# Kernel tuning notes

Hardware: AMD Instinct MI355X
Metric: run time of the kernel (lower is better)

Reference implementation:

```python
import jax, jax.numpy as jnp
import numpy as np

B, IMG, D, HEADS, L, PC, PF, OUT = 8, 128, 128, 4, 2, 8, 4, 32
HC = IMG // PC; NC = HC * HC          # 16x16 -> 256 coarse tokens
HF = IMG // PF; NF = HF * HF          # 32x32 -> 1024 fine tokens


def _ln(x, g, b):
    m = x.mean(-1, keepdims=True)
    v = x.var(-1, keepdims=True)
    return (x - m) * jax.lax.rsqrt(v + 1e-5) * g + b


def _conv(x, w, b, pad):
    y = jax.lax.conv_general_dilated(x, w, (1, 1), ((pad, pad), (pad, pad)),
                                     dimension_numbers=('NCHW', 'OIHW', 'NCHW'))
    return y + b[None, :, None, None]


def _bilinear_ac(x, oh, ow):  # F.interpolate(mode='bilinear', align_corners=True)
    _, _, H, W = x.shape
    ys = jnp.linspace(0.0, H - 1.0, oh)
    xs = jnp.linspace(0.0, W - 1.0, ow)
    y0 = jnp.floor(ys).astype(jnp.int32); y1 = jnp.minimum(y0 + 1, H - 1); wy = (ys - y0)[:, None]
    x0 = jnp.floor(xs).astype(jnp.int32); x1 = jnp.minimum(x0 + 1, W - 1); wx = (xs - x0)[None, :]
    g = lambda yi, xi: x[:, :, yi][:, :, :, xi]
    return (g(y0, x0) * (1 - wy) * (1 - wx) + g(y0, x1) * (1 - wy) * wx
            + g(y1, x0) * wy * (1 - wx) + g(y1, x1) * wy * wx)


def _patchify(x, p):  # F.unfold with kernel=stride=p, in_chans=1
    b, _, h, w = x.shape
    return x.reshape(b, h // p, p, w // p, p).transpose(0, 1, 3, 2, 4).reshape(b, (h // p) * (w // p), p * p)


def _forward(x, Wpc, bpc, Wpf, bpf, type_embed, ln1_g, ln1_b, Wqkv, Wo, bo,
             ln2_g, ln2_b, W1, b1, W2, b2, dWc, dbc, dWf, dbf, fW1, fb1, fW2, fb2):
    Bx = x.shape[0]
    # ---- multi-scale patch embed ----
    coarse = _patchify(x, PC) @ Wpc + bpc + type_embed[0]   # [B,NC,D]
    fine = _patchify(x, PF) @ Wpf + bpf                     # [B,NF,D]
    # ---- edge map: sobel -> avgpool(4) -> threshold at per-image mean ----
    gray = x.mean(1, keepdims=True)
    kx = jnp.array([[[[-1, 0, 1], [-2, 0, 2], [-1, 0, 1]]]], x.dtype)
    ky = jnp.array([[[[-1, -2, -1], [0, 0, 0], [1, 2, 1]]]], x.dtype)
    sx = _conv(gray, kx, jnp.zeros((1,), x.dtype), 1)
    sy = _conv(gray, ky, jnp.zeros((1,), x.dtype), 1)
    e = jnp.sqrt(sx ** 2 + sy ** 2)
    e = e.reshape(Bx, 1, IMG // 4, 4, IMG // 4, 4).mean((3, 5))  # [B,1,32,32] == fine grid
    mask_flat = (e > e.mean((2, 3), keepdims=True)).reshape(Bx, NF)
    # ---- static-shape analogue of per-sample masked gather + pad_sequence:
    # stable sort puts edge tokens first (original pixel order preserved), pads are zeros
    order = jnp.argsort(jnp.logical_not(mask_flat), axis=1, stable=True)   # [B,NF]
    mask_sorted = jnp.take_along_axis(mask_flat, order, 1)
    fine_sorted = jnp.take_along_axis(fine, order[..., None], 1) * mask_sorted[..., None]
    fine_sorted = fine_sorted + type_embed[1]   # type embed added to pads too (as in torch)
    tokens = jnp.concatenate([coarse, fine_sorted], axis=1)   # [B,N,D]
    N = NC + NF
    hd = D // HEADS
    scale = hd ** -0.5
    # ---- encoder blocks (pre-LN attn + MLP, irregular-token path) ----
    for l in range(L):
        y = _ln(tokens, ln1_g[l], ln1_b[l])
        qkv = (y @ Wqkv[l]).reshape(Bx, N, 3, HEADS, hd).transpose(2, 0, 3, 1, 4)
        q, k, v = qkv[0], qkv[1], qkv[2]
        attn = jax.nn.softmax(jnp.einsum('bhqd,bhkd->bhqk', q, k) * scale, axis=-1)
        o = jnp.einsum('bhqk,bhkd->bhqd', attn, v).transpose(0, 2, 1, 3).reshape(Bx, N, D)
        tokens = tokens + o @ Wo[l] + bo[l]
        y = _ln(tokens, ln2_g[l], ln2_b[l])
        tokens = tokens + jax.nn.gelu(y @ W1[l] + b1[l], approximate=False) @ W2[l] + b2[l]
    # ---- multi-scale decoder ----
    c = (tokens[:, :NC] @ dWc + dbc).reshape(Bx, HC, HC, 1).transpose(0, 3, 1, 2)
    c_up = _bilinear_ac(c, OUT, OUT)
    feats = (tokens[:, NC:] @ dWf + dbf) * mask_sorted[..., None]   # pads stay zero
    inv = jnp.argsort(order, axis=1)                                # scatter back to pixel order
    f_flat = jnp.take_along_axis(feats, inv[..., None], 1)          # [B,NF,1]
    f_map = f_flat.reshape(Bx, HF, HF, 1).transpose(0, 3, 1, 2)
    f_up = _bilinear_ac(f_map, OUT, OUT)
    fused = jnp.concatenate([c_up, f_up], axis=1)
    h = jax.nn.relu(_conv(fused, fW1, fb1, 1))
    return _conv(h, fW2, fb2, 1)   # [B,1,32,32]


def setup_inputs() -> dict:
    key = jax.random.key(0)
    ks = jax.random.split(key, 16)
    n = lambda k, shape: jax.random.normal(k, shape, jnp.float32) * 0.02
    z = lambda *shape: jnp.zeros(shape, jnp.float32)
    return {
        'x': jax.random.normal(ks[0], (B, 1, IMG, IMG), jnp.float32),
        'Wpc': n(ks[1], (PC * PC, D)), 'bpc': z(D),
        'Wpf': n(ks[2], (PF * PF, D)), 'bpf': z(D),
        'type_embed': n(ks[3], (2, D)),
        'ln1_g': jnp.ones((L, D), jnp.float32), 'ln1_b': z(L, D),
        'Wqkv': n(ks[4], (L, D, 3 * D)),
        'Wo': n(ks[5], (L, D, D)), 'bo': z(L, D),
        'ln2_g': jnp.ones((L, D), jnp.float32), 'ln2_b': z(L, D),
        'W1': n(ks[6], (L, D, 2 * D)), 'b1': z(L, 2 * D),
        'W2': n(ks[7], (L, 2 * D, D)), 'b2': z(L, D),
        'dWc': n(ks[8], (D, 1)), 'dbc': z(1),
        'dWf': n(ks[9], (D, 1)), 'dbf': z(1),
        'fW1': n(ks[10], (2, 2, 3, 3)) * 10.0, 'fb1': z(2),
        'fW2': n(ks[11], (1, 2, 3, 3)) * 10.0, 'fb2': z(1),
    }


def reference(x, Wpc, bpc, Wpf, bpf, type_embed, ln1_g, ln1_b, Wqkv, Wo, bo,
              ln2_g, ln2_b, W1, b1, W2, b2, dWc, dbc, dWf, dbf, fW1, fb1, fW2, fb2):
    return _forward(x, Wpc, bpc, Wpf, bpf, type_embed, ln1_g, ln1_b, Wqkv, Wo, bo,
                    ln2_g, ln2_b, W1, b1, W2, b2, dWc, dbc, dWf, dbf, fW1, fb1, fW2, fb2)
```

## Files before the change

### kernel.cpp

```cpp
#include <hip/hip_runtime.h>
#include <math.h>

#define Bx 8
#define IMG 128
#define DD 128
#define HEADS 4
#define LL 2
#define PCc 8
#define PFf 4
#define HCc 16
#define NCc 256
#define HFf 32
#define NFf 1024
#define NTOK 1280
#define HD 32
#define SPLIT 4
#define NQT 20

typedef __attribute__((ext_vector_type(8))) short short8;
typedef __attribute__((ext_vector_type(4))) float f32x4;

__device__ __forceinline__ short f2bf(float f) {
  unsigned u = __builtin_bit_cast(unsigned, f);
  u += 0x7FFF + ((u >> 16) & 1);
  return (short)(u >> 16);
}
__device__ __forceinline__ float bf2f(short s) {
  unsigned u = ((unsigned)(unsigned short)s) << 16;
  return __builtin_bit_cast(float, u);
}

__global__ __launch_bounds__(128) void k_coarse(const float* __restrict__ x,
    const float* __restrict__ Wpc, const float* __restrict__ bpc,
    const float* __restrict__ te, float* __restrict__ tokens) {
  int blk = blockIdx.x;
  int b = blk / NCc, t = blk % NCc;
  int hc = t / HCc, wc = t % HCc;
  int d = threadIdx.x;
  __shared__ float patch[PCc * PCc];
  if (d < PCc * PCc) {
    int pi = d / PCc, pj = d % PCc;
    patch[d] = x[(b * IMG + hc * PCc + pi) * IMG + wc * PCc + pj];
  }
  __syncthreads();
  float acc = bpc[d] + te[d];
  #pragma unroll 8
  for (int i = 0; i < PCc * PCc; ++i) acc += patch[i] * Wpc[i * DD + d];
  tokens[(size_t)(b * NTOK + t) * DD + d] = acc;
}

__global__ __launch_bounds__(256) void k_sobel(const float* __restrict__ x,
    float* __restrict__ e) {
  int blk = blockIdx.x;
  int b = blk >> 6, tile = blk & 63;
  int ty = tile >> 3, tx = tile & 7;
  int t = threadIdx.x;
  int ly = t >> 4, lx = t & 15;
  int py = ty * 16 + ly, px = tx * 16 + lx;
  const float* img = x + (size_t)b * IMG * IMG;
  float v[3][3];
  #pragma unroll
  for (int ky = 0; ky < 3; ++ky)
    #pragma unroll
    for (int kx = 0; kx < 3; ++kx) {
      int yy = py + ky - 1, xx = px + kx - 1;
      v[ky][kx] = (yy >= 0 && yy < IMG && xx >= 0 && xx < IMG)
                      ? img[yy * IMG + xx] : 0.f;
    }
  float gx = -v[0][0] + v[0][2] - 2.f * v[1][0] + 2.f * v[1][2] - v[2][0] + v[2][2];
  float gy = -v[0][0] - 2.f * v[0][1] - v[0][2] + v[2][0] + 2.f * v[2][1] + v[2][2];
  __shared__ float sm[256];
  sm[t] = sqrtf(gx * gx + gy * gy);
  __syncthreads();
  if (t < 16) {
    int cy = t >> 2, cx = t & 3;
    float s = 0.f;
    #pragma unroll
    for (int dy = 0; dy < 4; ++dy)
      #pragma unroll
      for (int dx = 0; dx < 4; ++dx) s += sm[(cy * 4 + dy) * 16 + cx * 4 + dx];
    e[b * NFf + (ty * 4 + cy) * 32 + tx * 4 + cx] = s * (1.f / 16.f);
  }
}

__global__ __launch_bounds__(1024) void k_edge_sort(const float* __restrict__ e,
    int* __restrict__ order, int* __restrict__ inv, float* __restrict__ msort) {
  int b = blockIdx.x;
  int t = threadIdx.x;
  int lane = t & 63, wave = t >> 6;
  float ev = e[b * NFf + t];
  __shared__ float wsum[16];
  __shared__ int wcnt[16];
  float r = ev;
  #pragma unroll
  for (int o = 32; o > 0; o >>= 1) r += __shfl_xor(r, o, 64);
  if (lane == 0) wsum[wave] = r;
  __syncthreads();
  float tot = 0.f;
  #pragma unroll
  for (int i = 0; i < 16; ++i) tot += wsum[i];
  float mean = tot * (1.f / 1024.f);
  int m = (ev > mean) ? 1 : 0;
  unsigned long long bal = __ballot(m);
  if (lane == 0) wcnt[wave] = __popcll(bal);
  __syncthreads();
  int wbase = 0, total = 0;
  #pragma unroll
  for (int i = 0; i < 16; ++i) {
    int c = wcnt[i];
    if (i < wave) wbase += c;
    total += c;
  }
  unsigned long long below = (lane == 63) ? ~0ULL : ((1ULL << (lane + 1)) - 1);
  int incl = __popcll(bal & below);
  int eb = wbase + incl - m;
  int pos = m ? eb : (total + t - eb);
  order[b * NFf + pos] = t;
  inv[b * NFf + t] = pos;
  msort[b * NFf + pos] = (float)m;
}

__global__ __launch_bounds__(128) void k_fine(const float* __restrict__ x,
    const float* __restrict__ Wpf, const float* __restrict__ bpf,
    const float* __restrict__ te, const int* __restrict__ inv,
    const float* __restrict__ msort, float* __restrict__ tokens) {
  int blk = blockIdx.x;
  int b = blk / NFf, t = blk % NFf;
  int hf = t / HFf, wf = t % HFf;
  int d = threadIdx.x;
  __shared__ float patch[PFf * PFf];
  if (d < PFf * PFf) {
    int pi = d / PFf, pj = d % PFf;
    patch[d] = x[(b * IMG + hf * PFf + pi) * IMG + wf * PFf + pj];
  }
  __syncthreads();
  float acc = bpf[d];
  #pragma unroll
  for (int i = 0; i < PFf * PFf; ++i) acc += patch[i] * Wpf[i * DD + d];
  int pos = inv[b * NFf + t];
  float mk = msort[b * NFf + pos];
  tokens[(size_t)(b * NTOK + NCc + pos) * DD + d] = acc * mk + te[DD + d];
}

__global__ __launch_bounds__(256) void k_prep_w(const float* __restrict__ Wqkv,
    const float* __restrict__ Wo, const float* __restrict__ W1,
    const float* __restrict__ W2, short* __restrict__ WtQKV,
    short* __restrict__ WtO, short* __restrict__ Wt1, short* __restrict__ Wt2) {
  int idx = blockIdx.x * 256 + threadIdx.x;
  int l = idx / 131072, r = idx % 131072;
  const float* src; short* dst; int N, off;
  if (r < 49152)      { src = Wqkv + l * 49152; dst = WtQKV + l * 49152; N = 384; off = r; }
  else if (r < 65536) { src = Wo + l * 16384;  dst = WtO + l * 16384;  N = 128; off = r - 49152; }
  else if (r < 98304) { src = W1 + l * 32768;  dst = Wt1 + l * 32768;  N = 256; off = r - 65536; }
  else                { src = W2 + l * 32768;  dst = Wt2 + l * 32768;  N = 128; off = r - 98304; }
  int k = off / N, n = off % N;
  int K = (r >= 98304) ? 256 : 128;
  dst[(size_t)n * K + k] = f2bf(src[off]);
}

__global__ __launch_bounds__(256) void k_ln_bf16(const float* __restrict__ inp,
    const float* __restrict__ g, const float* __restrict__ bb,
    short* __restrict__ outp) {
  int row = blockIdx.x * 4 + (threadIdx.x >> 6);
  int lane = threadIdx.x & 63;
  float2 v = ((const float2*)(inp + (size_t)row * DD))[lane];
  float s = v.x + v.y;
  #pragma unroll
  for (int o = 32; o > 0; o >>= 1) s += __shfl_xor(s, o, 64);
  float mean = s * (1.f / 128.f);
  float cx = v.x - mean, cy = v.y - mean;
  float q = cx * cx + cy * cy;
  #pragma unroll
  for (int o = 32; o > 0; o >>= 1) q += __shfl_xor(q, o, 64);
  float rstd = rsqrtf(q * (1.f / 128.f) + 1e-5f);
  float2 gg = ((const float2*)g)[lane];
  float2 bv = ((const float2*)bb)[lane];
  int p = (int)(unsigned short)f2bf(cx * rstd * gg.x + bv.x)
        | ((int)(unsigned short)f2bf(cy * rstd * gg.y + bv.y) << 16);
  ((int*)(outp + (size_t)row * DD))[lane] = p;
}

__global__ __launch_bounds__(256) void k_gemm_mfma(const short* __restrict__ A,
    const short* __restrict__ Wt, const float* __restrict__ bias,
    float* __restrict__ Cf, short* __restrict__ Cb, int K, int N, int do_gelu) {
  __shared__ short Alds[64 * 128];
  __shared__ short Blds[64 * 128];
  int row0 = blockIdx.x * 64, col0 = blockIdx.y * 64;
  int t = threadIdx.x;
  int lane = t & 63, w = t >> 6;
  int m = lane & 15, quad = lane >> 4;
  int lrow = lane >> 4, jphys = lane & 15;
  f32x4 zero = {0.f, 0.f, 0.f, 0.f};
  f32x4 acc[4] = {zero, zero, zero, zero};

  for (int kb = 0; kb < K; kb += 128) {
    __syncthreads();
    #pragma unroll
    for (int j = 0; j < 4; ++j) {
      int c = j * 4 + w;
      int r = c * 4 + lrow;
      int jlog = jphys ^ (r & 15);
      __builtin_amdgcn_global_load_lds(
          (const unsigned*)&A[(size_t)(row0 + r) * K + kb + jlog * 8],
          (unsigned*)&Alds[c * 512], 16, 0, 0);
      __builtin_amdgcn_global_load_lds(
          (const unsigned*)&Wt[(size_t)(col0 + r) * K + kb + jlog * 8],
          (unsigned*)&Blds[c * 512], 16, 0, 0);
    }
    __syncthreads();
    #pragma unroll
    for (int ks = 0; ks < 4; ++ks) {
      int pc = ((quad + ks * 4) ^ m) * 8;
      short8 af = *(const short8*)&Alds[(w * 16 + m) * 128 + pc];
      #pragma unroll
      for (int nt = 0; nt < 4; ++nt) {
        short8 bf = *(const short8*)&Blds[(nt * 16 + m) * 128 + pc];
        acc[nt] = __builtin_amdgcn_mfma_f32_16x16x32_bf16(af, bf, acc[nt], 0, 0, 0);
      }
    }
  }
  #pragma unroll
  for (int nt = 0; nt < 4; ++nt) {
    int col = col0 + nt * 16 + m;
    float bv = bias ? bias[col] : 0.f;
    #pragma unroll
    for (int r = 0; r < 4; ++r) {
      int row = row0 + w * 16 + quad * 4 + r;
      float v = acc[nt][r] + bv;
      if (do_gelu) v = 0.5f * v * (1.f + erff(v * 0.70710678118654752f));
      if (Cf) Cf[(size_t)row * N + col] += v;
      else    Cb[(size_t)row * N + col] = f2bf(v);
    }
  }
}

__global__ __launch_bounds__(256) void k_gemm_wo(const short* __restrict__ Opart,
    const float* __restrict__ Lpart, const short* __restrict__ Wt,
    const float* __restrict__ bias, float* __restrict__ Cf) {
  __shared__ short Alds[64 * 136];
  __shared__ short Blds[64 * 128];
  int row0 = blockIdx.x * 64, col0 = blockIdx.y * 64;
  int b = row0 / NTOK, qt = (row0 / 64) % NQT;
  int t = threadIdx.x;
  int lane = t & 63, w = t >> 6;
  int m = lane & 15, quad = lane >> 4;
  int lrow = lane >> 4, jphys = lane & 15;
  f32x4 zero = {0.f, 0.f, 0.f, 0.f};
  f32x4 acc[4] = {zero, zero, zero, zero};

  #pragma unroll
  for (int it = 0; it < 4; ++it) {
    int idx = t + it * 256;
    int q = idx >> 4, j = idx & 15;
    int hh = j >> 2, dd = (j & 3) * 8;
    size_t pb = ((size_t)(b * HEADS + hh) * NQT + qt) * SPLIT;
    float L = Lpart[(pb + 0) * 64 + q] + Lpart[(pb + 1) * 64 + q]
            + Lpart[(pb + 2) * 64 + q] + Lpart[(pb + 3) * 64 + q];
    float o[8] = {0, 0, 0, 0, 0, 0, 0, 0};
    #pragma unroll
    for (int sk = 0; sk < SPLIT; ++sk) {
      short8 po = *(const short8*)&Opart[(pb + sk) * 2048 + q * 32 + dd];
      #pragma unroll
      for (int i = 0; i < 8; ++i) o[i] += bf2f(po[i]);
    }
    float rs = 1.f / L;
    short8 ov;
    #pragma unroll
    for (int i = 0; i < 8; ++i) ov[i] = f2bf(o[i] * rs);
    *(short8*)&Alds[q * 136 + j * 8] = ov;
  }
  #pragma unroll
  for (int j = 0; j < 4; ++j) {
    int c = j * 4 + w;
    int r = c * 4 + lrow;
    int jlog = jphys ^ (r & 15);
    __builtin_amdgcn_global_load_lds(
        (const unsigned*)&Wt[(size_t)(col0 + r) * 128 + jlog * 8],
        (unsigned*)&Blds[c * 512], 16, 0, 0);
  }
  __syncthreads();
  #pragma unroll
  for (int ks = 0; ks < 4; ++ks) {
    short8 af = *(const short8*)&Alds[(w * 16 + m) * 136 + quad * 8 + ks * 32];
    int pc = ((quad + ks * 4) ^ m) * 8;
    #pragma unroll
    for (int nt = 0; nt < 4; ++nt) {
      short8 bf = *(const short8*)&Blds[(nt * 16 + m) * 128 + pc];
      acc[nt] = __builtin_amdgcn_mfma_f32_16x16x32_bf16(af, bf, acc[nt], 0, 0, 0);
    }
  }
  #pragma unroll
  for (int nt = 0; nt < 4; ++nt) {
    int col = col0 + nt * 16 + m;
    float bv = bias[col];
    #pragma unroll
    for (int r = 0; r < 4; ++r) {
      int row = row0 + w * 16 + quad * 4 + r;
      Cf[(size_t)row * DD + col] += acc[nt][r] + bv;
    }
  }
}

__global__ __launch_bounds__(256) void k_attn4(const short* __restrict__ qkv,
    short* __restrict__ Opart, float* __restrict__ Lpart) {
  __shared__ short Ks[64 * 32];
  __shared__ short Vt[32 * 74];
  __shared__ short Pl[4][16 * 74];

  int sk = blockIdx.x % SPLIT;
  int qt = (blockIdx.x / SPLIT) % NQT;
  int h  = (blockIdx.x / (SPLIT * NQT)) % HEADS;
  int b  = blockIdx.x / (SPLIT * NQT * HEADS);
  int t = threadIdx.x;
  int lane = t & 63, w = t >> 6;
  int m = lane & 15, quad = lane >> 4;
  int q0 = qt * 64 + w * 16;

  const float scale = 0.17677669529663687f;
  short8 qraw = *(const short8*)(qkv + ((size_t)(b * NTOK) + q0 + m) * 384 + h * HD + quad * 8);
  short8 qf;
  #pragma unroll
  for (int j = 0; j < 8; ++j) qf[j] = f2bf(bf2f(qraw[j]) * scale);

  f32x4 zero = {0.f, 0.f, 0.f, 0.f};
  f32x4 Oacc[2] = {zero, zero};
  float psum[4] = {0.f, 0.f, 0.f, 0.f};

  int skey = t >> 2, sdseg = t & 3;
  int jlogK = sdseg ^ ((skey >> 1) & 3);
  const short* kstage = qkv + ((size_t)(b * NTOK) + skey) * 384 + 128 + h * HD + jlogK * 8;
  const short* vstage = qkv + ((size_t)(b * NTOK) + skey) * 384 + 256 + h * HD + sdseg * 8;
  int kswz = (quad ^ ((m >> 1) & 3)) * 8;

  for (int s = sk * 5; s < sk * 5 + 5; ++s) {
    __syncthreads();
    __builtin_amdgcn_global_load_lds((const unsigned*)(kstage + (size_t)s * 64 * 384),
                                     (unsigned*)&Ks[w * 512], 16, 0, 0);
    short8 vf = *(const short8*)(vstage + (size_t)s * 64 * 384);
    #pragma unroll
    for (int j = 0; j < 8; ++j) Vt[(sdseg * 8 + j) * 74 + skey] = vf[j];
    __syncthreads();

    f32x4 sc[4];
    #pragma unroll
    for (int ct = 0; ct < 4; ++ct) {
      short8 kfrag = *(const short8*)&Ks[(ct * 16 + m) * 32 + kswz];
      sc[ct] = __builtin_amdgcn_mfma_f32_16x16x32_bf16(qf, kfrag, zero, 0, 0, 0);
    }
    #pragma unroll
    for (int ct = 0; ct < 4; ++ct)
      #pragma unroll
      for (int r = 0; r < 4; ++r) {
        float p = __expf(sc[ct][r]);
        unsigned u = __builtin_bit_cast(unsigned, p);
        psum[r] += __builtin_bit_cast(float, u & 0xffff0000u);
        Pl[w][(quad * 4 + r) * 74 + ct * 16 + m] = (short)(u >> 16);
      }
    #pragma unroll
    for (int ks = 0; ks < 2; ++ks) {
      short8 pfrag = *(const short8*)&Pl[w][m * 74 + ks * 32 + quad * 8];
      #pragma unroll
      for (int nt = 0; nt < 2; ++nt) {
        short8 vfrag = *(const short8*)&Vt[(nt * 16 + m) * 74 + ks * 32 + quad * 8];
        Oacc[nt] = __builtin_amdgcn_mfma_f32_16x16x32_bf16(pfrag, vfrag, Oacc[nt], 0, 0, 0);
      }
    }
  }
  #pragma unroll
  for (int r = 0; r < 4; ++r) {
    float ssum = psum[r];
    #pragma unroll
    for (int o = 1; o < 16; o <<= 1) ssum += __shfl_xor(ssum, o);
    int qloc = w * 16 + quad * 4 + r;
    #pragma unroll
    for (int nt = 0; nt < 2; ++nt)
      Opart[(size_t)blockIdx.x * 2048 + qloc * 32 + nt * 16 + m] = f2bf(Oacc[nt][r]);
    if (m == 0) Lpart[(size_t)blockIdx.x * 64 + qloc] = ssum;
  }
}

__global__ __launch_bounds__(1024) void k_coarse_dec(const float* __restrict__ tokens,
    const float* __restrict__ dWc, const float* __restrict__ dbc,
    float* __restrict__ c_up) {
  int b = blockIdx.x;
  int t = threadIdx.x;
  __shared__ float c[NCc];
  if (t < NCc) {
    const float* row = tokens + (size_t)(b * NTOK + t) * DD;
    float a = 0.f;
    for (int d = 0; d < DD; ++d) a += row[d] * dWc[d];
    c[t] = a + dbc[0];
  }
  __syncthreads();
  int oy = t >> 5, ox = t & 31;
  float ys = oy * (15.f / 31.f);
  float xs = ox * (15.f / 31.f);
  int y0 = (int)floorf(ys); int y1 = min(y0 + 1, 15); float wy = ys - (float)y0;
  int x0 = (int)floorf(xs); int x1 = min(x0 + 1, 15); float wx = xs - (float)x0;
  float v = c[y0 * 16 + x0] * (1.f - wy) * (1.f - wx)
          + c[y0 * 16 + x1] * (1.f - wy) * wx
          + c[y1 * 16 + x0] * wy * (1.f - wx)
          + c[y1 * 16 + x1] * wy * wx;
  c_up[b * 1024 + t] = v;
}

__global__ __launch_bounds__(256) void k_fine_dec(const float* __restrict__ tokens,
    const float* __restrict__ dWf, const float* __restrict__ dbf,
    const float* __restrict__ msort, const int* __restrict__ order,
    float* __restrict__ f_map) {
  int idx = blockIdx.x * 256 + threadIdx.x;
  int b = idx >> 10, j = idx & 1023;
  const float* row = tokens + (size_t)(b * NTOK + NCc + j) * DD;
  float a = 0.f;
  for (int d = 0; d < DD; ++d) a += row[d] * dWf[d];
  a = (a + dbf[0]) * msort[b * NFf + j];
  f_map[b * NFf + order[b * NFf + j]] = a;
}

__global__ __launch_bounds__(1024) void k_fuse_conv(const float* __restrict__ c_up,
    const float* __restrict__ f_map, const float* __restrict__ fW1,
    const float* __restrict__ fb1, const float* __restrict__ fW2,
    const float* __restrict__ fb2, float* __restrict__ outp) {
  int b = blockIdx.x;
  int t = threadIdx.x;
  int y = t >> 5, x = t & 31;
  __shared__ float fin[2][1024];
  __shared__ float hb[2][1024];
  fin[0][t] = c_up[b * 1024 + t];
  fin[1][t] = f_map[b * 1024 + t];
  __syncthreads();
  for (int oc = 0; oc < 2; ++oc) {
    float a = fb1[oc];
    #pragma unroll
    for (int ic = 0; ic < 2; ++ic)
      #pragma unroll
      for (int ky = 0; ky < 3; ++ky)
        #pragma unroll
        for (int kx = 0; kx < 3; ++kx) {
          int yy = y + ky - 1, xx = x + kx - 1;
          float v = (yy >= 0 && yy < 32 && xx >= 0 && xx < 32)
                        ? fin[ic][yy * 32 + xx] : 0.f;
          a += v * fW1[((oc * 2 + ic) * 3 + ky) * 3 + kx];
        }
    hb[oc][t] = fmaxf(a, 0.f);
  }
  __syncthreads();
  float a = fb2[0];
  #pragma unroll
  for (int ic = 0; ic < 2; ++ic)
    #pragma unroll
    for (int ky = 0; ky < 3; ++ky)
      #pragma unroll
      for (int kx = 0; kx < 3; ++kx) {
        int yy = y + ky - 1, xx = x + kx - 1;
        float v = (yy >= 0 && yy < 32 && xx >= 0 && xx < 32)
                      ? hb[ic][yy * 32 + xx] : 0.f;
        a += v * fW2[(ic * 3 + ky) * 3 + kx];
      }
  outp[b * 1024 + t] = a;
}

extern "C" void kernel_launch(void* const* d_in, const int* in_sizes, int n_in,
                              void* d_out, int out_size, void* d_ws, size_t ws_size,
                              hipStream_t stream) {
  const float* x    = (const float*)d_in[0];
  const float* Wpc  = (const float*)d_in[1];
  const float* bpc  = (const float*)d_in[2];
  const float* Wpf  = (const float*)d_in[3];
  const float* bpf  = (const float*)d_in[4];
  const float* te   = (const float*)d_in[5];
  const float* ln1g = (const float*)d_in[6];
  const float* ln1b = (const float*)d_in[7];
  const float* Wqkv = (const float*)d_in[8];
  const float* Wo   = (const float*)d_in[9];
  const float* bo   = (const float*)d_in[10];
  const float* ln2g = (const float*)d_in[11];
  const float* ln2b = (const float*)d_in[12];
  const float* W1   = (const float*)d_in[13];
  const float* b1   = (const float*)d_in[14];
  const float* W2   = (const float*)d_in[15];
  const float* b2   = (const float*)d_in[16];
  const float* dWc  = (const float*)d_in[17];
  const float* dbc  = (const float*)d_in[18];
  const float* dWf  = (const float*)d_in[19];
  const float* dbf  = (const float*)d_in[20];
  const float* fW1  = (const float*)d_in[21];
  const float* fb1  = (const float*)d_in[22];
  const float* fW2  = (const float*)d_in[23];
  const float* fb2  = (const float*)d_in[24];

  char* ws = (char*)d_ws;
  float* tokens = (float*)ws;                 ws += 1310720 * 4;
  short* ybuf   = (short*)ws;                 ws += 1310720 * 2;
  short* qkvb   = (short*)ws;                 ws += 3932160 * 2;
  short* hbuf   = (short*)ws;                 ws += 2621440 * 2;
  short* Opart  = (short*)ws;                 ws += (size_t)(Bx * HEADS * NQT * SPLIT) * 2048 * 2;
  float* Lpart  = (float*)ws;                 ws += (size_t)(Bx * HEADS * NQT * SPLIT) * 64 * 4;
  short* WtQKV  = (short*)ws;                 ws += 98304 * 2;
  short* WtO    = (short*)ws;                 ws += 32768 * 2;
  short* Wt1    = (short*)ws;                 ws += 65536 * 2;
  short* Wt2    = (short*)ws;                 ws += 65536 * 2;
  float* ebuf   = (float*)ws;                 ws += 8192 * 4;
  float* msort  = (float*)ws;                 ws += 8192 * 4;
  float* c_up   = (float*)ws;                 ws += 8192 * 4;
  float* f_map  = (float*)ws;                 ws += 8192 * 4;
  int*   order  = (int*)ws;                   ws += 8192 * 4;
  int*   inv    = (int*)ws;                   ws += 8192 * 4;

  const int M = Bx * NTOK;

  k_prep_w<<<1024, 256, 0, stream>>>(Wqkv, Wo, W1, W2, WtQKV, WtO, Wt1, Wt2);
  k_sobel<<<Bx * 64, 256, 0, stream>>>(x, ebuf);
  k_coarse<<<Bx * NCc, 128, 0, stream>>>(x, Wpc, bpc, te, tokens);
  k_edge_sort<<<Bx, 1024, 0, stream>>>(ebuf, order, inv, msort);
  k_fine<<<Bx * NFf, 128, 0, stream>>>(x, Wpf, bpf, te, inv, msort, tokens);

  for (int l = 0; l < LL; ++l) {
    k_ln_bf16<<<M / 4, 256, 0, stream>>>(tokens, ln1g + l * DD, ln1b + l * DD, ybuf);
    k_gemm_mfma<<<dim3(M / 64, 384 / 64), 256, 0, stream>>>(
        ybuf, WtQKV + (size_t)l * 49152, nullptr, nullptr, qkvb, 128, 384, 0);
    k_attn4<<<Bx * HEADS * NQT * SPLIT, 256, 0, stream>>>(qkvb, Opart, Lpart);
    k_gemm_wo<<<dim3(M / 64, 2), 256, 0, stream>>>(
        Opart, Lpart, WtO + (size_t)l * 16384, bo + l * DD, tokens);
    k_ln_bf16<<<M / 4, 256, 0, stream>>>(tokens, ln2g + l * DD, ln2b + l * DD, ybuf);
    k_gemm_mfma<<<dim3(M / 64, 256 / 64), 256, 0, stream>>>(
        ybuf, Wt1 + (size_t)l * 32768, b1 + l * 256, nullptr, hbuf, 128, 256, 1);
    k_gemm_mfma<<<dim3(M / 64, 128 / 64), 256, 0, stream>>>(
        hbuf, Wt2 + (size_t)l * 32768, b2 + l * DD, tokens, nullptr, 256, 128, 0);
  }

  k_coarse_dec<<<Bx, 1024, 0, stream>>>(tokens, dWc, dbc, c_up);
  k_fine_dec<<<Bx * NFf / 256, 256, 0, stream>>>(tokens, dWf, dbf, msort, order, f_map);
  k_fuse_conv<<<Bx, 1024, 0, stream>>>(c_up, f_map, fW1, fb1, fW2, fb2, (float*)d_out);
}
```

Baseline: 258.1 us.

## Double-buffer K/V tiles in attention and prefetch Wo weights earlier

```diff
diff --git a/kernel.cpp b/kernel.cpp
--- a/kernel.cpp
+++ b/kernel.cpp
@@ -249,6 +249,15 @@
   f32x4 acc[4] = {zero, zero, zero, zero};
 
   #pragma unroll
+  for (int j = 0; j < 4; ++j) {
+    int c = j * 4 + w;
+    int r = c * 4 + lrow;
+    int jlog = jphys ^ (r & 15);
+    __builtin_amdgcn_global_load_lds(
+        (const unsigned*)&Wt[(size_t)(col0 + r) * 128 + jlog * 8],
+        (unsigned*)&Blds[c * 512], 16, 0, 0);
+  }
+  #pragma unroll
   for (int it = 0; it < 4; ++it) {
     int idx = t + it * 256;
     int q = idx >> 4, j = idx & 15;
@@ -269,15 +278,6 @@
     for (int i = 0; i < 8; ++i) ov[i] = f2bf(o[i] * rs);
     *(short8*)&Alds[q * 136 + j * 8] = ov;
   }
-  #pragma unroll
-  for (int j = 0; j < 4; ++j) {
-    int c = j * 4 + w;
-    int r = c * 4 + lrow;
-    int jlog = jphys ^ (r & 15);
-    __builtin_amdgcn_global_load_lds(
-        (const unsigned*)&Wt[(size_t)(col0 + r) * 128 + jlog * 8],
-        (unsigned*)&Blds[c * 512], 16, 0, 0);
-  }
   __syncthreads();
   #pragma unroll
   for (int ks = 0; ks < 4; ++ks) {
@@ -301,10 +301,10 @@
   }
 }
 
-__global__ __launch_bounds__(256) void k_attn4(const short* __restrict__ qkv,
+__global__ __launch_bounds__(256) void k_attn5(const short* __restrict__ qkv,
     short* __restrict__ Opart, float* __restrict__ Lpart) {
-  __shared__ short Ks[64 * 32];
-  __shared__ short Vt[32 * 74];
+  __shared__ short Ks[2][64 * 32];
+  __shared__ short Vt[2][32 * 74];
   __shared__ short Pl[4][16 * 74];
 
   int sk = blockIdx.x % SPLIT;
@@ -331,20 +331,32 @@
   const short* kstage = qkv + ((size_t)(b * NTOK) + skey) * 384 + 128 + h * HD + jlogK * 8;
   const short* vstage = qkv + ((size_t)(b * NTOK) + skey) * 384 + 256 + h * HD + sdseg * 8;
   int kswz = (quad ^ ((m >> 1) & 3)) * 8;
-
-  for (int s = sk * 5; s < sk * 5 + 5; ++s) {
-    __syncthreads();
-    __builtin_amdgcn_global_load_lds((const unsigned*)(kstage + (size_t)s * 64 * 384),
-                                     (unsigned*)&Ks[w * 512], 16, 0, 0);
-    short8 vf = *(const short8*)(vstage + (size_t)s * 64 * 384);
-    #pragma unroll
-    for (int j = 0; j < 8; ++j) Vt[(sdseg * 8 + j) * 74 + skey] = vf[j];
-    __syncthreads();
+  int s0 = sk * 5;
+
+  __builtin_amdgcn_global_load_lds((const unsigned*)(kstage + (size_t)s0 * 64 * 384),
+                                   (unsigned*)&Ks[0][w * 512], 16, 0, 0);
+  {
+    short8 vf0 = *(const short8*)(vstage + (size_t)s0 * 64 * 384);
+    #pragma unroll
+    for (int j = 0; j < 8; ++j) Vt[0][(sdseg * 8 + j) * 74 + skey] = vf0[j];
+  }
+  short8 vfn = *(const short8*)(vstage + (size_t)(s0 + 1) * 64 * 384);
+  __syncthreads();
+
+  #pragma unroll
+  for (int s = 0; s < 5; ++s) {
+    int cur = s & 1, nxt = cur ^ 1;
+    if (s + 1 < 5)
+      __builtin_amdgcn_global_load_lds(
+          (const unsigned*)(kstage + (size_t)(s0 + s + 1) * 64 * 384),
+          (unsigned*)&Ks[nxt][w * 512], 16, 0, 0);
+    short8 vf2;
+    if (s + 2 < 5) vf2 = *(const short8*)(vstage + (size_t)(s0 + s + 2) * 64 * 384);
 
     f32x4 sc[4];
     #pragma unroll
     for (int ct = 0; ct < 4; ++ct) {
-      short8 kfrag = *(const short8*)&Ks[(ct * 16 + m) * 32 + kswz];
+      short8 kfrag = *(const short8*)&Ks[cur][(ct * 16 + m) * 32 + kswz];
       sc[ct] = __builtin_amdgcn_mfma_f32_16x16x32_bf16(qf, kfrag, zero, 0, 0, 0);
     }
     #pragma unroll
@@ -361,9 +373,15 @@
       short8 pfrag = *(const short8*)&Pl[w][m * 74 + ks * 32 + quad * 8];
       #pragma unroll
       for (int nt = 0; nt < 2; ++nt) {
-        short8 vfrag = *(const short8*)&Vt[(nt * 16 + m) * 74 + ks * 32 + quad * 8];
+        short8 vfrag = *(const short8*)&Vt[cur][(nt * 16 + m) * 74 + ks * 32 + quad * 8];
         Oacc[nt] = __builtin_amdgcn_mfma_f32_16x16x32_bf16(pfrag, vfrag, Oacc[nt], 0, 0, 0);
       }
+    }
+    if (s + 1 < 5) {
+      #pragma unroll
+      for (int j = 0; j < 8; ++j) Vt[nxt][(sdseg * 8 + j) * 74 + skey] = vfn[j];
+      vfn = vf2;
+      __syncthreads();
     }
   }
   #pragma unroll
@@ -519,7 +537,7 @@
     k_ln_bf16<<<M / 4, 256, 0, stream>>>(tokens, ln1g + l * DD, ln1b + l * DD, ybuf);
     k_gemm_mfma<<<dim3(M / 64, 384 / 64), 256, 0, stream>>>(
         ybuf, WtQKV + (size_t)l * 49152, nullptr, nullptr, qkvb, 128, 384, 0);
-    k_attn4<<<Bx * HEADS * NQT * SPLIT, 256, 0, stream>>>(qkvb, Opart, Lpart);
+    k_attn5<<<Bx * HEADS * NQT * SPLIT, 256, 0, stream>>>(qkvb, Opart, Lpart);
     k_gemm_wo<<<dim3(M / 64, 2), 256, 0, stream>>>(
         Opart, Lpart, WtO + (size_t)l * 16384, bo + l * DD, tokens);
     k_ln_bf16<<<M / 4, 256, 0, stream>>>(tokens, ln2g + l * DD, ln2b + l * DD, ybuf);
```

New measurement: 264.8 us. 2.6% more time.

## Fuse LayerNorm into GEMM prologue and merge prologue and decoder kernels

Applied to the files above, without the earlier changes.

```diff
diff --git a/kernel.cpp b/kernel.cpp
--- a/kernel.cpp
+++ b/kernel.cpp
@@ -30,56 +30,72 @@
   return __builtin_bit_cast(float, u);
 }
 
-__global__ __launch_bounds__(128) void k_coarse(const float* __restrict__ x,
+__global__ __launch_bounds__(256) void k_prologue(const float* __restrict__ x,
     const float* __restrict__ Wpc, const float* __restrict__ bpc,
-    const float* __restrict__ te, float* __restrict__ tokens) {
+    const float* __restrict__ te,
+    const float* __restrict__ Wqkv, const float* __restrict__ Wo,
+    const float* __restrict__ W1, const float* __restrict__ W2,
+    short* __restrict__ WtQKV, short* __restrict__ WtO,
+    short* __restrict__ Wt1, short* __restrict__ Wt2,
+    float* __restrict__ e, float* __restrict__ tokens) {
   int blk = blockIdx.x;
-  int b = blk / NCc, t = blk % NCc;
-  int hc = t / HCc, wc = t % HCc;
-  int d = threadIdx.x;
-  __shared__ float patch[PCc * PCc];
-  if (d < PCc * PCc) {
-    int pi = d / PCc, pj = d % PCc;
-    patch[d] = x[(b * IMG + hc * PCc + pi) * IMG + wc * PCc + pj];
-  }
-  __syncthreads();
-  float acc = bpc[d] + te[d];
-  #pragma unroll 8
-  for (int i = 0; i < PCc * PCc; ++i) acc += patch[i] * Wpc[i * DD + d];
-  tokens[(size_t)(b * NTOK + t) * DD + d] = acc;
-}
-
-__global__ __launch_bounds__(256) void k_sobel(const float* __restrict__ x,
-    float* __restrict__ e) {
-  int blk = blockIdx.x;
-  int b = blk >> 6, tile = blk & 63;
-  int ty = tile >> 3, tx = tile & 7;
   int t = threadIdx.x;
-  int ly = t >> 4, lx = t & 15;
-  int py = ty * 16 + ly, px = tx * 16 + lx;
-  const float* img = x + (size_t)b * IMG * IMG;
-  float v[3][3];
-  #pragma unroll
-  for (int ky = 0; ky < 3; ++ky)
-    #pragma unroll
-    for (int kx = 0; kx < 3; ++kx) {
-      int yy = py + ky - 1, xx = px + kx - 1;
-      v[ky][kx] = (yy >= 0 && yy < IMG && xx >= 0 && xx < IMG)
-                      ? img[yy * IMG + xx] : 0.f;
-    }
-  float gx = -v[0][0] + v[0][2] - 2.f * v[1][0] + 2.f * v[1][2] - v[2][0] + v[2][2];
-  float gy = -v[0][0] - 2.f * v[0][1] - v[0][2] + v[2][0] + 2.f * v[2][1] + v[2][2];
-  __shared__ float sm[256];
-  sm[t] = sqrtf(gx * gx + gy * gy);
-  __syncthreads();
-  if (t < 16) {
-    int cy = t >> 2, cx = t & 3;
-    float s = 0.f;
-    #pragma unroll
-    for (int dy = 0; dy < 4; ++dy)
-      #pragma unroll
-      for (int dx = 0; dx < 4; ++dx) s += sm[(cy * 4 + dy) * 16 + cx * 4 + dx];
-    e[b * NFf + (ty * 4 + cy) * 32 + tx * 4 + cx] = s * (1.f / 16.f);
+  if (blk < 1024) {
+    int idx = blk * 256 + t;
+    int l = idx / 131072, r = idx % 131072;
+    const float* src; short* dst; int N, off;
+    if (r < 49152)      { src = Wqkv + l * 49152; dst = WtQKV + l * 49152; N = 384; off = r; }
+    else if (r < 65536) { src = Wo + l * 16384;  dst = WtO + l * 16384;  N = 128; off = r - 49152; }
+    else if (r < 98304) { src = W1 + l * 32768;  dst = Wt1 + l * 32768;  N = 256; off = r - 65536; }
+    else                { src = W2 + l * 32768;  dst = Wt2 + l * 32768;  N = 128; off = r - 98304; }
+    int k = off / N, n = off % N;
+    int K = (r >= 98304) ? 256 : 128;
+    dst[(size_t)n * K + k] = f2bf(src[off]);
+  } else if (blk < 1536) {
+    int bt = blk - 1024;
+    int b = bt >> 6, tile = bt & 63;
+    int ty = tile >> 3, tx = tile & 7;
+    int ly = t >> 4, lx = t & 15;
+    int py = ty * 16 + ly, px = tx * 16 + lx;
+    const float* img = x + (size_t)b * IMG * IMG;
+    float v[3][3];
+    #pragma unroll
+    for (int ky = 0; ky < 3; ++ky)
+      #pragma unroll
+      for (int kx = 0; kx < 3; ++kx) {
+        int yy = py + ky - 1, xx = px + kx - 1;
+        v[ky][kx] = (yy >= 0 && yy < IMG && xx >= 0 && xx < IMG)
+                        ? img[yy * IMG + xx] : 0.f;
+      }
+    float gx = -v[0][0] + v[0][2] - 2.f * v[1][0] + 2.f * v[1][2] - v[2][0] + v[2][2];
+    float gy = -v[0][0] - 2.f * v[0][1] - v[0][2] + v[2][0] + 2.f * v[2][1] + v[2][2];
+    __shared__ float sm[256];
+    sm[t] = sqrtf(gx * gx + gy * gy);
+    __syncthreads();
+    if (t < 16) {
+      int cy = t >> 2, cx = t & 3;
+      float s = 0.f;
+      #pragma unroll
+      for (int dy = 0; dy < 4; ++dy)
+        #pragma unroll
+        for (int dx = 0; dx < 4; ++dx) s += sm[(cy * 4 + dy) * 16 + cx * 4 + dx];
+      e[b * NFf + (ty * 4 + cy) * 32 + tx * 4 + cx] = s * (1.f / 16.f);
+    }
+  } else {
+    int bt = (blk - 1536) * 2 + (t >> 7);
+    int b = bt / NCc, tok = bt % NCc;
+    int hc = tok / HCc, wc = tok % HCc;
+    int half = t >> 7, d = t & 127;
+    __shared__ float patch[2][PCc * PCc];
+    if (d < PCc * PCc) {
+      int pi = d / PCc, pj = d % PCc;
+      patch[half][d] = x[(b * IMG + hc * PCc + pi) * IMG + wc * PCc + pj];
+    }
+    __syncthreads();
+    float acc = bpc[d] + te[d];
+    #pragma unroll 8
+    for (int i = 0; i < PCc * PCc; ++i) acc += patch[half][i] * Wpc[i * DD + d];
+    tokens[(size_t)(b * NTOK + tok) * DD + d] = acc;
   }
 }
 
@@ -142,46 +158,9 @@
   tokens[(size_t)(b * NTOK + NCc + pos) * DD + d] = acc * mk + te[DD + d];
 }
 
-__global__ __launch_bounds__(256) void k_prep_w(const float* __restrict__ Wqkv,
-    const float* __restrict__ Wo, const float* __restrict__ W1,
-    const float* __restrict__ W2, short* __restrict__ WtQKV,
-    short* __restrict__ WtO, short* __restrict__ Wt1, short* __restrict__ Wt2) {
-  int idx = blockIdx.x * 256 + threadIdx.x;
-  int l = idx / 131072, r = idx % 131072;
-  const float* src; short* dst; int N, off;
-  if (r < 49152)      { src = Wqkv + l * 49152; dst = WtQKV + l * 49152; N = 384; off = r; }
-  else if (r < 65536) { src = Wo + l * 16384;  dst = WtO + l * 16384;  N = 128; off = r - 49152; }
-  else if (r < 98304) { src = W1 + l * 32768;  dst = Wt1 + l * 32768;  N = 256; off = r - 65536; }
-  else                { src = W2 + l * 32768;  dst = Wt2 + l * 32768;  N = 128; off = r - 98304; }
-  int k = off / N, n = off % N;
-  int K = (r >= 98304) ? 256 : 128;
-  dst[(size_t)n * K + k] = f2bf(src[off]);
-}
-
-__global__ __launch_bounds__(256) void k_ln_bf16(const float* __restrict__ inp,
-    const float* __restrict__ g, const float* __restrict__ bb,
-    short* __restrict__ outp) {
-  int row = blockIdx.x * 4 + (threadIdx.x >> 6);
-  int lane = threadIdx.x & 63;
-  float2 v = ((const float2*)(inp + (size_t)row * DD))[lane];
-  float s = v.x + v.y;
-  #pragma unroll
-  for (int o = 32; o > 0; o >>= 1) s += __shfl_xor(s, o, 64);
-  float mean = s * (1.f / 128.f);
-  float cx = v.x - mean, cy = v.y - mean;
-  float q = cx * cx + cy * cy;
-  #pragma unroll
-  for (int o = 32; o > 0; o >>= 1) q += __shfl_xor(q, o, 64);
-  float rstd = rsqrtf(q * (1.f / 128.f) + 1e-5f);
-  float2 gg = ((const float2*)g)[lane];
-  float2 bv = ((const float2*)bb)[lane];
-  int p = (int)(unsigned short)f2bf(cx * rstd * gg.x + bv.x)
-        | ((int)(unsigned short)f2bf(cy * rstd * gg.y + bv.y) << 16);
-  ((int*)(outp + (size_t)row * DD))[lane] = p;
-}
-
-__global__ __launch_bounds__(256) void k_gemm_mfma(const short* __restrict__ A,
+__global__ __launch_bounds__(256) void k_gemm_mfma(const void* __restrict__ Av,
     const short* __restrict__ Wt, const float* __restrict__ bias,
+    const float* __restrict__ lng, const float* __restrict__ lnb,
     float* __restrict__ Cf, short* __restrict__ Cb, int K, int N, int do_gelu) {
   __shared__ short Alds[64 * 128];
   __shared__ short Blds[64 * 128];
@@ -195,17 +174,66 @@
 
   for (int kb = 0; kb < K; kb += 128) {
     __syncthreads();
-    #pragma unroll
-    for (int j = 0; j < 4; ++j) {
-      int c = j * 4 + w;
-      int r = c * 4 + lrow;
-      int jlog = jphys ^ (r & 15);
-      __builtin_amdgcn_global_load_lds(
-          (const unsigned*)&A[(size_t)(row0 + r) * K + kb + jlog * 8],
-          (unsigned*)&Alds[c * 512], 16, 0, 0);
-      __builtin_amdgcn_global_load_lds(
-          (const unsigned*)&Wt[(size_t)(col0 + r) * K + kb + jlog * 8],
-          (unsigned*)&Blds[c * 512], 16, 0, 0);
+    if (lng) {
+      #pragma unroll
+      for (int j = 0; j < 4; ++j) {
+        int c = j * 4 + w;
+        int r = c * 4 + lrow;
+        int jlog = jphys ^ (r & 15);
+        __builtin_amdgcn_global_load_lds(
+            (const unsigned*)&Wt[(size_t)(col0 + r) * 128 + jlog * 8],
+            (unsigned*)&Blds[c * 512], 16, 0, 0);
+      }
+      int r = t >> 2, seg = t & 3;
+      const float* arow = (const float*)Av + (size_t)(row0 + r) * 128 + seg * 32;
+      float vv[32];
+      float s = 0.f, q = 0.f;
+      #pragma unroll
+      for (int j = 0; j < 8; ++j) {
+        float4 u = ((const float4*)arow)[j];
+        vv[j * 4 + 0] = u.x; vv[j * 4 + 1] = u.y;
+        vv[j * 4 + 2] = u.z; vv[j * 4 + 3] = u.w;
+        s += u.x + u.y + u.z + u.w;
+        q += u.x * u.x + u.y * u.y + u.z * u.z + u.w * u.w;
+      }
+      s += __shfl_xor(s, 1); s += __shfl_xor(s, 2);
+      q += __shfl_xor(q, 1); q += __shfl_xor(q, 2);
+      float mean = s * (1.f / 128.f);
+      float var = q * (1.f / 128.f) - mean * mean;
+      float rstd = rsqrtf(var + 1e-5f);
+      #pragma unroll
+      for (int j8 = 0; j8 < 4; ++j8) {
+        float4 g1 = ((const float4*)(lng + seg * 32))[j8 * 2];
+        float4 g2 = ((const float4*)(lng + seg * 32))[j8 * 2 + 1];
+        float4 b1 = ((const float4*)(lnb + seg * 32))[j8 * 2];
+        float4 b2 = ((const float4*)(lnb + seg * 32))[j8 * 2 + 1];
+        short8 o;
+        o[0] = f2bf((vv[j8 * 8 + 0] - mean) * rstd * g1.x + b1.x);
+        o[1] = f2bf((vv[j8 * 8 + 1] - mean) * rstd * g1.y + b1.y);
+        o[2] = f2bf((vv[j8 * 8 + 2] - mean) * rstd * g1.z + b1.z);
+        o[3] = f2bf((vv[j8 * 8 + 3] - mean) * rstd * g1.w + b1.w);
+        o[4] = f2bf((vv[j8 * 8 + 4] - mean) * rstd * g2.x + b2.x);
+        o[5] = f2bf((vv[j8 * 8 + 5] - mean) * rstd * g2.y + b2.y);
+        o[6] = f2bf((vv[j8 * 8 + 6] - mean) * rstd * g2.z + b2.z);
+        o[7] = f2bf((vv[j8 * 8 + 7] - mean) * rstd * g2.w + b2.w);
+        int jlog = seg * 4 + j8;
+        int jphy = jlog ^ (r & 15);
+        *(short8*)&Alds[r * 128 + jphy * 8] = o;
+      }
+    } else {
+      const short* A = (const short*)Av;
+      #pragma unroll
+      for (int j = 0; j < 4; ++j) {
+        int c = j * 4 + w;
+        int r = c * 4 + lrow;
+        int jlog = jphys ^ (r & 15);
+        __builtin_amdgcn_global_load_lds(
+            (const unsigned*)&A[(size_t)(row0 + r) * K + kb + jlog * 8],
+            (unsigned*)&Alds[c * 512], 16, 0, 0);
+        __builtin_amdgcn_global_load_lds(
+            (const unsigned*)&Wt[(size_t)(col0 + r) * K + kb + jlog * 8],
+            (unsigned*)&Blds[c * 512], 16, 0, 0);
+      }
     }
     __syncthreads();
     #pragma unroll
@@ -249,6 +277,15 @@
   f32x4 acc[4] = {zero, zero, zero, zero};
 
   #pragma unroll
+  for (int j = 0; j < 4; ++j) {
+    int c = j * 4 + w;
+    int r = c * 4 + lrow;
+    int jlog = jphys ^ (r & 15);
+    __builtin_amdgcn_global_load_lds(
+        (const unsigned*)&Wt[(size_t)(col0 + r) * 128 + jlog * 8],
+        (unsigned*)&Blds[c * 512], 16, 0, 0);
+  }
+  #pragma unroll
   for (int it = 0; it < 4; ++it) {
     int idx = t + it * 256;
     int q = idx >> 4, j = idx & 15;
@@ -269,15 +306,6 @@
     for (int i = 0; i < 8; ++i) ov[i] = f2bf(o[i] * rs);
     *(short8*)&Alds[q * 136 + j * 8] = ov;
   }
-  #pragma unroll
-  for (int j = 0; j < 4; ++j) {
-    int c = j * 4 + w;
-    int r = c * 4 + lrow;
-    int jlog = jphys ^ (r & 15);
-    __builtin_amdgcn_global_load_lds(
-        (const unsigned*)&Wt[(size_t)(col0 + r) * 128 + jlog * 8],
-        (unsigned*)&Blds[c * 512], 16, 0, 0);
-  }
   __syncthreads();
   #pragma unroll
   for (int ks = 0; ks < 4; ++ks) {
@@ -379,55 +407,54 @@
   }
 }
 
-__global__ __launch_bounds__(1024) void k_coarse_dec(const float* __restrict__ tokens,
+__global__ __launch_bounds__(1024) void k_decoder(const float* __restrict__ tokens,
     const float* __restrict__ dWc, const float* __restrict__ dbc,
-    float* __restrict__ c_up) {
+    const float* __restrict__ dWf, const float* __restrict__ dbf,
+    const float* __restrict__ msort, const int* __restrict__ order,
+    const float* __restrict__ fW1, const float* __restrict__ fb1,
+    const float* __restrict__ fW2, const float* __restrict__ fb2,
+    float* __restrict__ outp) {
   int b = blockIdx.x;
   int t = threadIdx.x;
-  __shared__ float c[NCc];
+  __shared__ float cmap[NCc];
+  __shared__ float fmap[1024];
+  __shared__ float cup[1024];
+  __shared__ float hb[2][1024];
+  {
+    const float* row = tokens + (size_t)(b * NTOK + NCc + t) * DD;
+    float a = 0.f;
+    #pragma unroll 8
+    for (int d4 = 0; d4 < 32; ++d4) {
+      float4 u = ((const float4*)row)[d4];
+      float4 wv = ((const float4*)dWf)[d4];
+      a += u.x * wv.x + u.y * wv.y + u.z * wv.z + u.w * wv.w;
+    }
+    a = (a + dbf[0]) * msort[b * NFf + t];
+    fmap[order[b * NFf + t]] = a;
+  }
   if (t < NCc) {
     const float* row = tokens + (size_t)(b * NTOK + t) * DD;
     float a = 0.f;
-    for (int d = 0; d < DD; ++d) a += row[d] * dWc[d];
-    c[t] = a + dbc[0];
-  }
-  __syncthreads();
-  int oy = t >> 5, ox = t & 31;
-  float ys = oy * (15.f / 31.f);
-  float xs = ox * (15.f / 31.f);
-  int y0 = (int)floorf(ys); int y1 = min(y0 + 1, 15); float wy = ys - (float)y0;
-  int x0 = (int)floorf(xs); int x1 = min(x0 + 1, 15); float wx = xs - (float)x0;
-  float v = c[y0 * 16 + x0] * (1.f - wy) * (1.f - wx)
-          + c[y0 * 16 + x1] * (1.f - wy) * wx
-          + c[y1 * 16 + x0] * wy * (1.f - wx)
-          + c[y1 * 16 + x1] * wy * wx;
-  c_up[b * 1024 + t] = v;
-}
-
-__global__ __launch_bounds__(256) void k_fine_dec(const float* __restrict__ tokens,
-    const float* __restrict__ dWf, const float* __restrict__ dbf,
-    const float* __restrict__ msort, const int* __restrict__ order,
-    float* __restrict__ f_map) {
-  int idx = blockIdx.x * 256 + threadIdx.x;
-  int b = idx >> 10, j = idx & 1023;
-  const float* row = tokens + (size_t)(b * NTOK + NCc + j) * DD;
-  float a = 0.f;
-  for (int d = 0; d < DD; ++d) a += row[d] * dWf[d];
-  a = (a + dbf[0]) * msort[b * NFf + j];
-  f_map[b * NFf + order[b * NFf + j]] = a;
-}
-
-__global__ __launch_bounds__(1024) void k_fuse_conv(const float* __restrict__ c_up,
-    const float* __restrict__ f_map, const float* __restrict__ fW1,
-    const float* __restrict__ fb1, const float* __restrict__ fW2,
-    const float* __restrict__ fb2, float* __restrict__ outp) {
-  int b = blockIdx.x;
-  int t = threadIdx.x;
+    #pragma unroll 8
+    for (int d4 = 0; d4 < 32; ++d4) {
+      float4 u = ((const float4*)row)[d4];
+      float4 wv = ((const float4*)dWc)[d4];
+      a += u.x * wv.x + u.y * wv.y + u.z * wv.z + u.w * wv.w;
+    }
+    cmap[t] = a + dbc[0];
+  }
+  __syncthreads();
   int y = t >> 5, x = t & 31;
-  __shared__ float fin[2][1024];
-  __shared__ float hb[2][1024];
-  fin[0][t] = c_up[b * 1024 + t];
-  fin[1][t] = f_map[b * 1024 + t];
+  {
+    float ys = y * (15.f / 31.f);
+    float xs = x * (15.f / 31.f);
+    int y0 = (int)floorf(ys); int y1 = min(y0 + 1, 15); float wy = ys - (float)y0;
+    int x0 = (int)floorf(xs); int x1 = min(x0 + 1, 15); float wx = xs - (float)x0;
+    cup[t] = cmap[y0 * 16 + x0] * (1.f - wy) * (1.f - wx)
+           + cmap[y0 * 16 + x1] * (1.f - wy) * wx
+           + cmap[y1 * 16 + x0] * wy * (1.f - wx)
+           + cmap[y1 * 16 + x1] * wy * wx;
+  }
   __syncthreads();
   for (int oc = 0; oc < 2; ++oc) {
     float a = fb1[oc];
@@ -438,8 +465,9 @@
         #pragma unroll
         for (int kx = 0; kx < 3; ++kx) {
           int yy = y + ky - 1, xx = x + kx - 1;
-          float v = (yy >= 0 && yy < 32 && xx >= 0 && xx < 32)
-                        ? fin[ic][yy * 32 + xx] : 0.f;
+          float v = 0.f;
+          if (yy >= 0 && yy < 32 && xx >= 0 && xx < 32)
+            v = ic == 0 ? cup[yy * 32 + xx] : fmap[yy * 32 + xx];
           a += v * fW1[((oc * 2 + ic) * 3 + ky) * 3 + kx];
         }
     hb[oc][t] = fmaxf(a, 0.f);
@@ -491,7 +519,6 @@
 
   char* ws = (char*)d_ws;
   float* tokens = (float*)ws;                 ws += 1310720 * 4;
-  short* ybuf   = (short*)ws;                 ws += 1310720 * 2;
   short* qkvb   = (short*)ws;                 ws += 3932160 * 2;
   short* hbuf   = (short*)ws;                 ws += 2621440 * 2;
   short* Opart  = (short*)ws;                 ws += (size_t)(Bx * HEADS * NQT * SPLIT) * 2048 * 2;
@@ -502,34 +529,31 @@
   short* Wt2    = (short*)ws;                 ws += 65536 * 2;
   float* ebuf   = (float*)ws;                 ws += 8192 * 4;
   float* msort  = (float*)ws;                 ws += 8192 * 4;
-  float* c_up   = (float*)ws;                 ws += 8192 * 4;
-  float* f_map  = (float*)ws;                 ws += 8192 * 4;
   int*   order  = (int*)ws;                   ws += 8192 * 4;
   int*   inv    = (int*)ws;                   ws += 8192 * 4;
 
   const int M = Bx * NTOK;
 
-  k_prep_w<<<1024, 256, 0, stream>>>(Wqkv, Wo, W1, W2, WtQKV, WtO, Wt1, Wt2);
-  k_sobel<<<Bx * 64, 256, 0, stream>>>(x, ebuf);
-  k_coarse<<<Bx * NCc, 128, 0, stream>>>(x, Wpc, bpc, te, tokens);
+  k_prologue<<<2560, 256, 0, stream>>>(x, Wpc, bpc, te, Wqkv, Wo, W1, W2,
+                                       WtQKV, WtO, Wt1, Wt2, ebuf, tokens);
   k_edge_sort<<<Bx, 1024, 0, stream>>>(ebuf, order, inv, msort);
   k_fine<<<Bx * NFf, 128, 0, stream>>>(x, Wpf, bpf, te, inv, msort, tokens);
 
   for (int l = 0; l < LL; ++l) {
-    k_ln_bf16<<<M / 4, 256, 0, stream>>>(tokens, ln1g + l * DD, ln1b + l * DD, ybuf);
     k_gemm_mfma<<<dim3(M / 64, 384 / 64), 256, 0, stream>>>(
-        ybuf, WtQKV + (size_t)l * 49152, nullptr, nullptr, qkvb, 128, 384, 0);
+        tokens, WtQKV + (size_t)l * 49152, nullptr,
+        ln1g + l * DD, ln1b + l * DD, nullptr, qkvb, 128, 384, 0);
     k_attn4<<<Bx * HEADS * NQT * SPLIT, 256, 0, stream>>>(qkvb, Opart, Lpart);
     k_gemm_wo<<<dim3(M / 64, 2), 256, 0, stream>>>(
         Opart, Lpart, WtO + (size_t)l * 16384, bo + l * DD, tokens);
-    k_ln_bf16<<<M / 4, 256, 0, stream>>>(tokens, ln2g + l * DD, ln2b + l * DD, ybuf);
     k_gemm_mfma<<<dim3(M / 64, 256 / 64), 256, 0, stream>>>(
-        ybuf, Wt1 + (size_t)l * 32768, b1 + l * 256, nullptr, hbuf, 128, 256, 1);
+        tokens, Wt1 + (size_t)l * 32768, b1 + l * 256,
+        ln2g + l * DD, ln2b + l * DD, nullptr, hbuf, 128, 256, 1);
     k_gemm_mfma<<<dim3(M / 64, 128 / 64), 256, 0, stream>>>(
-        hbuf, Wt2 + (size_t)l * 32768, b2 + l * DD, tokens, nullptr, 256, 128, 0);
-  }
-
-  k_coarse_dec<<<Bx, 1024, 0, stream>>>(tokens, dWc, dbc, c_up);
-  k_fine_dec<<<Bx * NFf / 256, 256, 0, stream>>>(tokens, dWf, dbf, msort, order, f_map);
-  k_fuse_conv<<<Bx, 1024, 0, stream>>>(c_up, f_map, fW1, fb1, fW2, fb2, (float*)d_out);
-}
+        hbuf, Wt2 + (size_t)l * 32768, b2 + l * DD,
+        nullptr, nullptr, tokens, nullptr, 256, 128, 0);
+  }
+
+  k_decoder<<<Bx, 1024, 0, stream>>>(tokens, dWc, dbc, dWf, dbf, msort, order,
+                                     fW1, fb1, fW2, fb2, (float*)d_out);
+}
```

Result: slower. 280.2 us (+8.5%).
